# Performance work log

Hardware: AMD Instinct MI355X
Metric: run time of the kernel (lower is better)

The kernel has to match this reference:

```python
import jax, jax.numpy as jnp
import numpy as np

NE, EW, TOP_K, T_D, MAXNNZ = 32, 2944, 4, 8, 256
ALPHA, LIMIT, ORIG = 1.702, 7.0, 2880
HID = 2048


def setup_inputs() -> dict:
    key = jax.random.key(0)
    ks = jax.random.split(key, 7)
    dt = jnp.float16
    hid = jax.random.normal(ks[0], (1, 1024, HID), dtype=dt)
    # rand_init() sets all params to torch.rand(...)/5 -> Uniform[0, 0.2)
    gate_w = (jax.random.uniform(ks[1], (NE, HID), dtype=dt) * 0.2).astype(dt)
    u = (jax.random.uniform(ks[2], (NE * EW, HID), dtype=dt) * 0.2).astype(dt)
    g = (jax.random.uniform(ks[3], (NE * EW, HID), dtype=dt) * 0.2).astype(dt)
    d = (jax.random.uniform(ks[4], (HID, NE * EW), dtype=dt) * 0.2).astype(dt)
    ub = (jax.random.uniform(ks[5], (NE * EW,), dtype=dt) * 0.2).astype(dt)
    gb = (jax.random.uniform(ks[6], (NE * EW,), dtype=dt) * 0.2).astype(dt)
    return {"hid": hid, "gate_w": gate_w, "u": u, "g": g, "d": d, "ub": ub, "gb": gb}


def _act(up, gate):
    # clamped GLU: gate clamped above, up clamped both sides; glu = g*sigmoid(alpha*g); (up+1)*glu
    gate = jnp.minimum(gate, LIMIT)
    up = jnp.clip(up, -LIMIT, LIMIT)
    glu = gate * jax.nn.sigmoid(gate * ALPHA)
    act = (up + 1.0) * glu
    return act.at[..., ORIG:].set(0)  # padded inter dims (2880..2944) zeroed


def _forward(hid, gate_w, u, g, d, ub, gb):
    B, S, H = hid.shape
    x = hid.reshape(-1, H)           # [bs, H]
    bs = x.shape[0]

    # --- routing: softmax -> top-k -> renormalize -> scatter to sparse weights ---
    logits = (x @ gate_w.T).astype(jnp.float32)          # [bs, NE]
    probs = jax.nn.softmax(logits, axis=1)
    vals, idx = jax.lax.top_k(probs, TOP_K)
    vals = vals / vals.sum(axis=1, keepdims=True)
    sparse_rw = jnp.zeros_like(probs).at[jnp.arange(bs)[:, None], idx].set(vals)
    rw = sparse_rw.astype(x.dtype)                        # [bs, NE]

    # --- expert selection: t_d dense experts + t_d sparse experts by load ---
    routing_n = jnp.count_nonzero(rw, axis=0)
    mask_c = jax.lax.top_k(routing_n, 2 * T_D)[1]         # [2*T_D]
    cd, cs = mask_c[:T_D], mask_c[T_D:]
    # top-MAXNNZ tokens per sparse expert
    mask_r = jax.lax.top_k(sparse_rw[:, cs].T, MAXNNZ)[1].T  # [MAXNNZ, T_D]

    U = u.reshape(NE, EW, H)
    G = g.reshape(NE, EW, H)
    UB = ub.reshape(NE, EW)
    GB = gb.reshape(NE, EW)
    D = d.reshape(H, NE, EW)

    # --- dense experts: every token runs through the t_d hottest experts ---
    up_d = jnp.einsum('nh,teh->nte', x, U[cd]) + UB[cd]   # [bs, T_D, EW]
    gt_d = jnp.einsum('nh,teh->nte', x, G[cd]) + GB[cd]
    act_d = _act(up_d, gt_d) * rw[:, cd][..., None]       # routing weight combine
    out = jnp.einsum('nte,hte->nh', act_d, D[:, cd])      # [bs, H]

    # --- sparse experts: gather top-MAXNNZ tokens, MLP, scatter-add back ---
    xs = x[mask_r]                                        # [M, T_D, H]
    up_s = jnp.einsum('mth,teh->mte', xs, U[cs]) + UB[cs]
    gt_s = jnp.einsum('mth,teh->mte', xs, G[cs]) + GB[cs]
    w_s = rw[mask_r, cs[None, :]]                         # [M, T_D]
    act_s = _act(up_s, gt_s) * w_s[..., None]
    contrib = jnp.einsum('mte,hte->mth', act_s, D[:, cs])  # [M, T_D, H]
    out = out.at[mask_r.reshape(-1)].add(contrib.reshape(-1, H))

    return out.reshape(B, S, H)


def reference(hid, gate_w, u, g, d, ub, gb):
    return _forward(hid, gate_w, u, g, d, ub, gb)
```

## Files before the change

kernel.cpp:

```cpp
#include <hip/hip_runtime.h>

#define HID 2048
#define NE_ 32
#define EW_ 2944
#define ORIG_ 2880
#define TOPK_ 4
#define MAXNNZ_ 256
#define BS_ 1024
#define NEWTOT (NE_*EW_)
#define LDSP 40

typedef unsigned short u16;
typedef _Float16 h8  __attribute__((ext_vector_type(8)));
typedef float  f32x4 __attribute__((ext_vector_type(4)));
typedef float  fv4   __attribute__((ext_vector_type(4)));

__device__ __forceinline__ u16 f2h_bits(float f){
  union{ _Float16 h; u16 u; } c; c.h = (_Float16)f; return c.u;
}
__device__ __forceinline__ float h2f_bits(u16 u){
  union{ _Float16 h; u16 u; } c; c.u = u; return (float)c.h;
}
__device__ __forceinline__ float f16q(float f){ return (float)(_Float16)f; }

__device__ __forceinline__ h8 cvt8(fv4 a, fv4 b){
  h8 r;
  r[0]=(_Float16)a[0]; r[1]=(_Float16)a[1]; r[2]=(_Float16)a[2]; r[3]=(_Float16)a[3];
  r[4]=(_Float16)b[0]; r[5]=(_Float16)b[1]; r[6]=(_Float16)b[2]; r[7]=(_Float16)b[3];
  return r;
}
__device__ __forceinline__ int ldsx(int row, int q8){ return row*LDSP + q8*8; }

__global__ __launch_bounds__(256) void k_xcvt(const float* __restrict__ x,
                                              u16* __restrict__ xh)
{
  const int base = (blockIdx.x*256 + threadIdx.x)*8;
  fv4 a = *(const fv4*)(x+base), b = *(const fv4*)(x+base+4);
  *(h8*)(xh+base) = cvt8(a,b);
}

__global__ __launch_bounds__(256) void k_gate(const float* __restrict__ x,
                                              const float* __restrict__ gw,
                                              float* __restrict__ rw,
                                              float* __restrict__ rwf,
                                              int* __restrict__ counts)
{
  __shared__ float slog[4][NE_];
  const int tid = threadIdx.x, wid = tid>>6, lane = tid&63;
  const int n = blockIdx.x*4 + wid;
  const float* xr = x + (size_t)n*HID + lane*32;
  float xf[32];
  #pragma unroll
  for (int i=0;i<8;i++){
    fv4 v = *(const fv4*)(xr + i*4);
    #pragma unroll
    for (int j=0;j<4;j++) xf[i*4+j] = v[j];
  }
  for (int e=0;e<NE_;e++){
    const float* gr = gw + (size_t)e*HID + lane*32;
    float p = 0.f;
    #pragma unroll
    for (int i=0;i<8;i++){
      fv4 v = *(const fv4*)(gr + i*4);
      #pragma unroll
      for (int j=0;j<4;j++) p += xf[i*4+j]*v[j];
    }
    #pragma unroll
    for (int s=32;s>0;s>>=1) p += __shfl_xor(p, s);
    if (lane==0) slog[wid][e] = f16q(p);
  }
  if (lane==0){
    float mx=-1e30f;
    for (int e=0;e<NE_;e++) mx = fmaxf(mx, slog[wid][e]);
    float pr[NE_]; float sum=0.f;
    for (int e=0;e<NE_;e++){ float v=__expf(slog[wid][e]-mx); pr[e]=v; sum+=v; }
    for (int e=0;e<NE_;e++) pr[e] = pr[e]/sum;
    int   idx[TOPK_]; float val[TOPK_]; bool used[NE_];
    for (int e=0;e<NE_;e++) used[e]=false;
    float vs=0.f;
    for (int k=0;k<TOPK_;k++){
      float best=-1.f; int bi=0;
      for (int e=0;e<NE_;e++) if(!used[e] && pr[e]>best){best=pr[e];bi=e;}
      used[bi]=true; idx[k]=bi; val[k]=best; vs+=best;
    }
    float* rwr  = rw  + (size_t)n*NE_;
    float* rwfr = rwf + (size_t)n*NE_;
    for (int k=0;k<TOPK_;k++){
      float vraw = val[k]/vs;
      float q = f16q(vraw);
      rwr[idx[k]]  = q;
      rwfr[idx[k]] = vraw;
      if (q!=0.f) atomicAdd(counts+idx[k], 1);
    }
  }
}

__global__ void k_rank(const int* __restrict__ counts, int* __restrict__ cdcs)
{
  if (threadIdx.x==0){
    int cnt[NE_]; bool used[NE_];
    for (int e=0;e<NE_;e++){ cnt[e]=counts[e]; used[e]=false; }
    for (int k=0;k<16;k++){
      int best=-1, bi=0;
      for (int e=0;e<NE_;e++) if(!used[e] && cnt[e]>best){best=cnt[e];bi=e;}
      used[bi]=true; cdcs[k]=bi;
    }
  }
}

__global__ __launch_bounds__(256) void k_lists(const float* __restrict__ rw,
                                               const float* __restrict__ rwf,
                                               const int* __restrict__ cdcs,
                                               int* __restrict__ tok_all,
                                               int* __restrict__ cnt_all,
                                               int* __restrict__ inv,
                                               int* __restrict__ invcnt)
{
  __shared__ float v[BS_];
  __shared__ int scnt;
  const int z = blockIdx.x;
  const int e = cdcs[z];
  const int tid = threadIdx.x;
  for (int i=tid;i<BS_;i+=256) tok_all[z*BS_+i] = 0;
  for (int i=tid;i<BS_;i+=256) v[i] = (z<8) ? rw[(size_t)i*NE_+e] : rwf[(size_t)i*NE_+e];
  if (tid==0) scnt = 0;
  __syncthreads();
  for (int i=tid;i<BS_;i+=256){
    bool take;
    if (z<8){
      take = (v[i]!=0.f);
    } else {
      float vi=v[i]; int r=0;
      for (int m=0;m<BS_;m++){
        float vm=v[m];
        r += (vm>vi) || (vm==vi && m<i);
      }
      take = (r<MAXNNZ_) && (rw[(size_t)i*NE_+e]!=0.f);
    }
    if (take){
      int slot = atomicAdd(&scnt,1);
      tok_all[z*BS_+slot] = i;
      int c = atomicAdd(&invcnt[i],1);
      inv[i*4+c] = (z<<16) | slot;
    }
  }
  __syncthreads();
  if (tid==0) cnt_all[z] = scnt;
}

__global__ __launch_bounds__(256) void k_fused(const u16* __restrict__ xh,
                                               const float* __restrict__ uw,
                                               const float* __restrict__ gww,
                                               const float* __restrict__ ub,
                                               const float* __restrict__ gb,
                                               const float* __restrict__ rw,
                                               const int* __restrict__ cdcs,
                                               const int* __restrict__ tok_all,
                                               const int* __restrict__ cnt_all,
                                               u16* __restrict__ act)
{
  const int z=blockIdx.z, bx=blockIdx.x, by=blockIdx.y;
  const int cnt = cnt_all[z];
  if (by*256 >= cnt) return;
  const int e = cdcs[z];
  __shared__ __align__(16) u16 ldsA[2][256*LDSP];
  __shared__ __align__(16) u16 ldsB[2][64*LDSP];
  const int tid=threadIdx.x, lane=tid&63, w=tid>>6;

  const int ar = tid>>2, ach = tid&3;
  const u16* ap[4];
  #pragma unroll
  for (int r=0;r<4;r++){
    const int tok = tok_all[z*BS_ + by*256 + ar + r*64];
    ap[r] = xh + (size_t)tok*HID + ach*8;
  }
  const int br = tid>>2;
  const float* bp = (br<32 ? uw  + ((size_t)e*EW_ + bx*32 + br)*HID
                           : gww + ((size_t)e*EW_ + bx*32 + (br-32))*HID) + ach*8;

  f32x4 au[4][2], ag[4][2];
  #pragma unroll
  for (int i=0;i<4;i++)
    #pragma unroll
    for (int j=0;j<2;j++)
      #pragma unroll
      for (int q=0;q<4;q++){ au[i][j][q]=0.f; ag[i][j][q]=0.f; }

  h8 rA[4];
  #pragma unroll
  for (int r=0;r<4;r++) rA[r] = *(const h8*)ap[r];
  fv4 rB0=*(const fv4*)bp, rB1=*(const fv4*)(bp+4);
  const int NK = HID/32;
  for (int kt=0; kt<NK; kt++){
    u16* A = ldsA[kt&1]; u16* B = ldsB[kt&1];
    #pragma unroll
    for (int r=0;r<4;r++) *(h8*)&A[ldsx(ar + r*64, ach)] = rA[r];
    *(h8*)&B[ldsx(br, ach)] = cvt8(rB0,rB1);
    if (kt+1<NK){
      const int k1=(kt+1)*32;
      #pragma unroll
      for (int r=0;r<4;r++) rA[r] = *(const h8*)(ap[r]+k1);
      rB0=*(const fv4*)(bp+k1); rB1=*(const fv4*)(bp+k1+4);
    }
    __syncthreads();
    const int kq = lane>>4;
    const u16* Ar = ldsA[kt&1]; const u16* Br = ldsB[kt&1];
    h8 af[4], fu[2], fg[2];
    #pragma unroll
    for (int m=0;m<4;m++) af[m] = *(const h8*)&Ar[ldsx(w*64+m*16+(lane&15), kq)];
    #pragma unroll
    for (int n2=0;n2<2;n2++){
      fu[n2] = *(const h8*)&Br[ldsx(n2*16+(lane&15), kq)];
      fg[n2] = *(const h8*)&Br[ldsx(32+n2*16+(lane&15), kq)];
    }
    #pragma unroll
    for (int m=0;m<4;m++)
      #pragma unroll
      for (int n2=0;n2<2;n2++){
        au[m][n2]=__builtin_amdgcn_mfma_f32_16x16x32_f16(af[m],fu[n2],au[m][n2],0,0,0);
        ag[m][n2]=__builtin_amdgcn_mfma_f32_16x16x32_f16(af[m],fg[n2],ag[m][n2],0,0,0);
      }
  }

  #pragma unroll
  for (int n2=0;n2<2;n2++){
    const int col = bx*32 + n2*16 + (lane&15);
    const float ubv = ub[(size_t)e*EW_ + col];
    const float gbv = gb[(size_t)e*EW_ + col];
    #pragma unroll
    for (int m=0;m<4;m++){
      #pragma unroll
      for (int j=0;j<4;j++){
        const int s = by*256 + w*64 + m*16 + (lane>>4)*4 + j;
        if (s < cnt){
          float upv = f16q(au[m][n2][j] + ubv);
          float gtv = f16q(ag[m][n2][j] + gbv);
          float wv = rw[(size_t)tok_all[z*BS_+s]*NE_ + e];
          float gc = fminf(gtv, 7.0f);
          float uc = fminf(fmaxf(upv,-7.0f),7.0f);
          float glu = gc * (1.f/(1.f+__expf(-gc*1.702f)));
          act[((size_t)z*BS_+s)*ORIG_ + col] = f2h_bits((uc+1.f)*glu*wv);
        }
      }
    }
  }
}

__global__ __launch_bounds__(256) void k_down(const u16* __restrict__ act,
                                              const float* __restrict__ dw,
                                              const int* __restrict__ cdcs,
                                              const int* __restrict__ cnt_all,
                                              u16* __restrict__ contrib)
{
  const int zz=blockIdx.z, bx=blockIdx.x, by=blockIdx.y;
  const int z = zz>>1, kh = zz&1;
  const int cnt = cnt_all[z];
  if (by*256 >= cnt) return;
  const int e = cdcs[z];
  __shared__ __align__(16) u16 ldsA[2][256*LDSP];
  __shared__ __align__(16) u16 ldsB[2][64*LDSP];
  const int tid=threadIdx.x, lane=tid&63, w=tid>>6;
  const int ar = tid>>2, ach = tid&3;
  const int kbase = kh*1440;

  const u16* ap[4];
  #pragma unroll
  for (int r=0;r<4;r++)
    ap[r] = act + ((size_t)z*BS_ + by*256 + ar + r*64)*ORIG_ + kbase + ach*8;
  const float* bp = dw + (size_t)(bx*64 + ar)*NEWTOT + (size_t)e*EW_ + kbase + ach*8;

  f32x4 acc[4][4];
  #pragma unroll
  for (int i=0;i<4;i++)
    #pragma unroll
    for (int j=0;j<4;j++)
      #pragma unroll
      for (int q=0;q<4;q++) acc[i][j][q]=0.f;

  h8 rA[4];
  #pragma unroll
  for (int r=0;r<4;r++) rA[r] = *(const h8*)ap[r];
  fv4 rB0=*(const fv4*)bp, rB1=*(const fv4*)(bp+4);
  const int NK = 1440/32;
  for (int kt=0; kt<NK; kt++){
    u16* A = ldsA[kt&1]; u16* B = ldsB[kt&1];
    #pragma unroll
    for (int r=0;r<4;r++) *(h8*)&A[ldsx(ar + r*64, ach)] = rA[r];
    *(h8*)&B[ldsx(ar, ach)] = cvt8(rB0,rB1);
    if (kt+1<NK){
      const int k1 = (kt+1)*32;
      #pragma unroll
      for (int r=0;r<4;r++) rA[r] = *(const h8*)(ap[r]+k1);
      rB0=*(const fv4*)(bp+k1); rB1=*(const fv4*)(bp+k1+4);
    }
    __syncthreads();
    const int kq = lane>>4;
    const u16* Ar = ldsA[kt&1]; const u16* Br = ldsB[kt&1];
    h8 af[4], bfr[4];
    #pragma unroll
    for (int m=0;m<4;m++)    af[m]  = *(const h8*)&Ar[ldsx(w*64+m*16+(lane&15), kq)];
    #pragma unroll
    for (int n2=0;n2<4;n2++) bfr[n2] = *(const h8*)&Br[ldsx(n2*16+(lane&15), kq)];
    #pragma unroll
    for (int m=0;m<4;m++)
      #pragma unroll
      for (int n2=0;n2<4;n2++)
        acc[m][n2]=__builtin_amdgcn_mfma_f32_16x16x32_f16(af[m],bfr[n2],acc[m][n2],0,0,0);
  }

  #pragma unroll
  for (int m=0;m<4;m++){
    #pragma unroll
    for (int j=0;j<4;j++){
      const int slot = by*256 + w*64 + m*16 + (lane>>4)*4 + j;
      if (slot < cnt){
        #pragma unroll
        for (int n2=0;n2<4;n2++){
          const int col = bx*64 + n2*16 + (lane&15);
          contrib[((size_t)zz*BS_ + slot)*HID + col] = f2h_bits(acc[m][n2][j]);
        }
      }
    }
  }
}

__global__ __launch_bounds__(256) void k_combine(const u16* __restrict__ contrib,
                                                 const int* __restrict__ inv,
                                                 const int* __restrict__ invcnt,
                                                 float* __restrict__ out)
{
  const int gid = blockIdx.x*256 + threadIdx.x;
  const int base = gid*8;
  const int n = base >> 11;
  const int h = base & 2047;
  float acc[8];
  #pragma unroll
  for (int q=0;q<8;q++) acc[q]=0.f;
  const int c = invcnt[n];
  for (int j=0;j<c;j++){
    const int code = inv[n*4+j];
    const int z = code>>16;
    const int slot = code & 0xFFFF;
    const u16* p = contrib + ((size_t)(z*2)*BS_ + slot)*HID + h;
    h8 v0 = *(const h8*)p;
    h8 v1 = *(const h8*)(p + (size_t)BS_*HID);
    #pragma unroll
    for (int q=0;q<8;q++) acc[q] += (float)v0[q] + (float)v1[q];
  }
  fv4 o0, o1;
  #pragma unroll
  for (int q=0;q<4;q++){ o0[q]=acc[q]; o1[q]=acc[4+q]; }
  *(fv4*)(out + base) = o0;
  *(fv4*)(out + base + 4) = o1;
}

extern "C" void kernel_launch(void* const* d_in, const int* in_sizes, int n_in,
                              void* d_out, int out_size, void* d_ws, size_t ws_size,
                              hipStream_t stream)
{
  const float* x  = (const float*)d_in[0];
  const float* gw = (const float*)d_in[1];
  const float* u  = (const float*)d_in[2];
  const float* g  = (const float*)d_in[3];
  const float* dw = (const float*)d_in[4];
  const float* ub = (const float*)d_in[5];
  const float* gb = (const float*)d_in[6];

  char* ws = (char*)d_ws;
  size_t off = 0;
  auto alloc = [&](size_t bytes)->void*{ void* p = ws + off; off += (bytes + 255) & ~(size_t)255; return p; };
  float* rw     = (float*)alloc((size_t)BS_*NE_*4);
  float* rwf    = (float*)alloc((size_t)BS_*NE_*4);
  int*   counts = (int*)  alloc(NE_*4);
  int*   invcnt = (int*)  alloc(BS_*4);
  size_t zero_span = off;
  int*   cdcs   = (int*)  alloc(16*4);
  int*   cnt_all= (int*)  alloc(16*4);
  int*   tok_all= (int*)  alloc((size_t)16*BS_*4);
  int*   inv    = (int*)  alloc((size_t)BS_*4*4);
  u16*   xh     = (u16*)  alloc((size_t)BS_*HID*2);
  u16*   act    = (u16*)  alloc((size_t)16*BS_*ORIG_*2);
  u16*   contrib= (u16*)  alloc((size_t)32*BS_*HID*2);
  if (off > ws_size) return;

  hipMemsetAsync(ws, 0, zero_span, stream);

  k_xcvt <<<BS_*HID/(256*8), 256, 0, stream>>>(x, xh);
  k_gate <<<BS_/4, 256, 0, stream>>>(x, gw, rw, rwf, counts);
  k_rank <<<1,     64,  0, stream>>>(counts, cdcs);
  k_lists<<<16,    256, 0, stream>>>(rw, rwf, cdcs, tok_all, cnt_all, inv, invcnt);

  k_fused<<<dim3(ORIG_/32, 4, 16), 256, 0, stream>>>(xh, u, g, ub, gb, rw,
                                                     cdcs, tok_all, cnt_all, act);
  k_down <<<dim3(HID/64, 4, 32), 256, 0, stream>>>(act, dw, cdcs, cnt_all, contrib);
  k_combine<<<BS_*HID/(256*8), 256, 0, stream>>>(contrib, inv, invcnt, (float*)d_out);
}
```

Baseline: 575.0 us.

## Load A tiles directly into LDS with swizzle and deepen B prefetch

The A operand (fp16 activations/tokens) in both the fused up/gate GEMM and the down GEMM is now copied from global memory straight into LDS with global_load_lds, skipping registers. The LDS layout is unpadded with an XOR swizzle on 16-byte chunks to avoid bank conflicts. The fp32 B weights get a two-deep register prefetch, and the barrier moves to the top of the loop. The aim is to cut VGPR pressure and ds_write traffic and hide more load latency. The risk is synchronisation: nothing explicitly waits for the async LDS loads (no vmcnt wait) before the barrier, so correctness relies on the compiler inserting one.

Measured after the change: 582.3 us. No clear change (+1.3%).

```diff
diff --git a/kernel.cpp b/kernel.cpp
--- a/kernel.cpp
+++ b/kernel.cpp
@@ -18,9 +18,6 @@
 __device__ __forceinline__ u16 f2h_bits(float f){
   union{ _Float16 h; u16 u; } c; c.h = (_Float16)f; return c.u;
 }
-__device__ __forceinline__ float h2f_bits(u16 u){
-  union{ _Float16 h; u16 u; } c; c.u = u; return (float)c.h;
-}
 __device__ __forceinline__ float f16q(float f){ return (float)(_Float16)f; }
 
 __device__ __forceinline__ h8 cvt8(fv4 a, fv4 b){
@@ -29,7 +26,10 @@
   r[4]=(_Float16)b[0]; r[5]=(_Float16)b[1]; r[6]=(_Float16)b[2]; r[7]=(_Float16)b[3];
   return r;
 }
-__device__ __forceinline__ int ldsx(int row, int q8){ return row*LDSP + q8*8; }
+__device__ __forceinline__ void gload16(const void* g, void* l){
+  __builtin_amdgcn_global_load_lds((const __attribute__((address_space(1))) void*)g,
+                                   (__attribute__((address_space(3))) void*)l, 16, 0, 0);
+}
 
 __global__ __launch_bounds__(256) void k_xcvt(const float* __restrict__ x,
                                               u16* __restrict__ xh)
@@ -163,16 +163,16 @@
   const int cnt = cnt_all[z];
   if (by*256 >= cnt) return;
   const int e = cdcs[z];
-  __shared__ __align__(16) u16 ldsA[2][256*LDSP];
+  __shared__ __align__(16) u16 ldsA[2][256*32];
   __shared__ __align__(16) u16 ldsB[2][64*LDSP];
   const int tid=threadIdx.x, lane=tid&63, w=tid>>6;
-
   const int ar = tid>>2, ach = tid&3;
+  const int swc = ach ^ (ar&3);
   const u16* ap[4];
   #pragma unroll
   for (int r=0;r<4;r++){
     const int tok = tok_all[z*BS_ + by*256 + ar + r*64];
-    ap[r] = xh + (size_t)tok*HID + ach*8;
+    ap[r] = xh + (size_t)tok*HID + swc*8;
   }
   const int br = tid>>2;
   const float* bp = (br<32 ? uw  + ((size_t)e*EW_ + bx*32 + br)*HID
@@ -186,32 +186,37 @@
       #pragma unroll
       for (int q=0;q<4;q++){ au[i][j][q]=0.f; ag[i][j][q]=0.f; }
 
-  h8 rA[4];
-  #pragma unroll
-  for (int r=0;r<4;r++) rA[r] = *(const h8*)ap[r];
-  fv4 rB0=*(const fv4*)bp, rB1=*(const fv4*)(bp+4);
   const int NK = HID/32;
+  #pragma unroll
+  for (int r=0;r<4;r++) gload16(ap[r], &ldsA[0][(r*64 + 16*w)*32]);
+  fv4 s0a=*(const fv4*)bp,      s0b=*(const fv4*)(bp+4);
+  fv4 s1a=*(const fv4*)(bp+32), s1b=*(const fv4*)(bp+36);
+  *(h8*)&ldsB[0][br*LDSP + ach*8] = cvt8(s0a,s0b);
+  s0a=*(const fv4*)(bp+64); s0b=*(const fv4*)(bp+68);
+
   for (int kt=0; kt<NK; kt++){
-    u16* A = ldsA[kt&1]; u16* B = ldsB[kt&1];
-    #pragma unroll
-    for (int r=0;r<4;r++) *(h8*)&A[ldsx(ar + r*64, ach)] = rA[r];
-    *(h8*)&B[ldsx(br, ach)] = cvt8(rB0,rB1);
+    __syncthreads();
+    const int cur=kt&1, nxt=cur^1;
     if (kt+1<NK){
       const int k1=(kt+1)*32;
-      #pragma unroll
-      for (int r=0;r<4;r++) rA[r] = *(const h8*)(ap[r]+k1);
-      rB0=*(const fv4*)(bp+k1); rB1=*(const fv4*)(bp+k1+4);
-    }
-    __syncthreads();
+      if (((kt+1)&1)==0) *(h8*)&ldsB[nxt][br*LDSP + ach*8] = cvt8(s0a,s0b);
+      else               *(h8*)&ldsB[nxt][br*LDSP + ach*8] = cvt8(s1a,s1b);
+      #pragma unroll
+      for (int r=0;r<4;r++) gload16(ap[r]+k1, &ldsA[nxt][(r*64 + 16*w)*32]);
+      const int k3 = (kt+3<NK ? kt+3 : NK-1)*32;
+      if (((kt+1)&1)==0){ s0a=*(const fv4*)(bp+k3); s0b=*(const fv4*)(bp+k3+4); }
+      else              { s1a=*(const fv4*)(bp+k3); s1b=*(const fv4*)(bp+k3+4); }
+    }
     const int kq = lane>>4;
-    const u16* Ar = ldsA[kt&1]; const u16* Br = ldsB[kt&1];
+    const int rch = (kq ^ (lane&3))*8;
     h8 af[4], fu[2], fg[2];
     #pragma unroll
-    for (int m=0;m<4;m++) af[m] = *(const h8*)&Ar[ldsx(w*64+m*16+(lane&15), kq)];
+    for (int m=0;m<4;m++)
+      af[m] = *(const h8*)&ldsA[cur][(w*64+m*16+(lane&15))*32 + rch];
     #pragma unroll
     for (int n2=0;n2<2;n2++){
-      fu[n2] = *(const h8*)&Br[ldsx(n2*16+(lane&15), kq)];
-      fg[n2] = *(const h8*)&Br[ldsx(32+n2*16+(lane&15), kq)];
+      fu[n2] = *(const h8*)&ldsB[cur][(   n2*16+(lane&15))*LDSP + kq*8];
+      fg[n2] = *(const h8*)&ldsB[cur][(32+n2*16+(lane&15))*LDSP + kq*8];
     }
     #pragma unroll
     for (int m=0;m<4;m++)
@@ -257,16 +262,17 @@
   const int cnt = cnt_all[z];
   if (by*256 >= cnt) return;
   const int e = cdcs[z];
-  __shared__ __align__(16) u16 ldsA[2][256*LDSP];
+  __shared__ __align__(16) u16 ldsA[2][256*32];
   __shared__ __align__(16) u16 ldsB[2][64*LDSP];
   const int tid=threadIdx.x, lane=tid&63, w=tid>>6;
   const int ar = tid>>2, ach = tid&3;
+  const int swc = ach ^ (ar&3);
   const int kbase = kh*1440;
 
   const u16* ap[4];
   #pragma unroll
   for (int r=0;r<4;r++)
-    ap[r] = act + ((size_t)z*BS_ + by*256 + ar + r*64)*ORIG_ + kbase + ach*8;
+    ap[r] = act + ((size_t)z*BS_ + by*256 + ar + r*64)*ORIG_ + kbase + swc*8;
   const float* bp = dw + (size_t)(bx*64 + ar)*NEWTOT + (size_t)e*EW_ + kbase + ach*8;
 
   f32x4 acc[4][4];
@@ -277,30 +283,36 @@
       #pragma unroll
       for (int q=0;q<4;q++) acc[i][j][q]=0.f;
 
-  h8 rA[4];
-  #pragma unroll
-  for (int r=0;r<4;r++) rA[r] = *(const h8*)ap[r];
-  fv4 rB0=*(const fv4*)bp, rB1=*(const fv4*)(bp+4);
   const int NK = 1440/32;
+  #pragma unroll
+  for (int r=0;r<4;r++) gload16(ap[r], &ldsA[0][(r*64 + 16*w)*32]);
+  fv4 s0a=*(const fv4*)bp,      s0b=*(const fv4*)(bp+4);
+  fv4 s1a=*(const fv4*)(bp+32), s1b=*(const fv4*)(bp+36);
+  *(h8*)&ldsB[0][ar*LDSP + ach*8] = cvt8(s0a,s0b);
+  s0a=*(const fv4*)(bp+64); s0b=*(const fv4*)(bp+68);
+
   for (int kt=0; kt<NK; kt++){
-    u16* A = ldsA[kt&1]; u16* B = ldsB[kt&1];
-    #pragma unroll
-    for (int r=0;r<4;r++) *(h8*)&A[ldsx(ar + r*64, ach)] = rA[r];
-    *(h8*)&B[ldsx(ar, ach)] = cvt8(rB0,rB1);
+    __syncthreads();
+    const int cur=kt&1, nxt=cur^1;
     if (kt+1<NK){
-      const int k1 = (kt+1)*32;
-      #pragma unroll
-      for (int r=0;r<4;r++) rA[r] = *(const h8*)(ap[r]+k1);
-      rB0=*(const fv4*)(bp+k1); rB1=*(const fv4*)(bp+k1+4);
-    }
-    __syncthreads();
+      const int k1=(kt+1)*32;
+      if (((kt+1)&1)==0) *(h8*)&ldsB[nxt][ar*LDSP + ach*8] = cvt8(s0a,s0b);
+      else               *(h8*)&ldsB[nxt][ar*LDSP + ach*8] = cvt8(s1a,s1b);
+      #pragma unroll
+      for (int r=0;r<4;r++) gload16(ap[r]+k1, &ldsA[nxt][(r*64 + 16*w)*32]);
+      const int k3 = (kt+3<NK ? kt+3 : NK-1)*32;
+      if (((kt+1)&1)==0){ s0a=*(const fv4*)(bp+k3); s0b=*(const fv4*)(bp+k3+4); }
+      else              { s1a=*(const fv4*)(bp+k3); s1b=*(const fv4*)(bp+k3+4); }
+    }
     const int kq = lane>>4;
-    const u16* Ar = ldsA[kt&1]; const u16* Br = ldsB[kt&1];
+    const int rch = (kq ^ (lane&3))*8;
     h8 af[4], bfr[4];
     #pragma unroll
-    for (int m=0;m<4;m++)    af[m]  = *(const h8*)&Ar[ldsx(w*64+m*16+(lane&15), kq)];
-    #pragma unroll
-    for (int n2=0;n2<4;n2++) bfr[n2] = *(const h8*)&Br[ldsx(n2*16+(lane&15), kq)];
+    for (int m=0;m<4;m++)
+      af[m] = *(const h8*)&ldsA[cur][(w*64+m*16+(lane&15))*32 + rch];
+    #pragma unroll
+    for (int n2=0;n2<4;n2++)
+      bfr[n2] = *(const h8*)&ldsB[cur][(n2*16+(lane&15))*LDSP + kq*8];
     #pragma unroll
     for (int m=0;m<4;m++)
       #pragma unroll
```

## Load MFMA fragments directly from global memory, dropping LDS staging and barriers

Applied to the files above, without the earlier changes.

Both the fused up/gate GEMM and the down-projection GEMM stop staging tiles through double-buffered shared memory. Each lane now loads its own MFMA fragments straight from global memory into registers, prefetching the next k-step in registers, and the per-step __syncthreads goes away. Previously the weight tile was loaded once per block and shared by all four waves through LDS. Now each wave fetches it itself, so weight reads from L2/global rise about fourfold in exchange for removing barriers and LDS traffic.

Result: slower. 985.2 us (+71.4%).

```diff
diff --git a/kernel.cpp b/kernel.cpp
--- a/kernel.cpp
+++ b/kernel.cpp
@@ -8,7 +8,6 @@
 #define MAXNNZ_ 256
 #define BS_ 1024
 #define NEWTOT (NE_*EW_)
-#define LDSP 40
 
 typedef unsigned short u16;
 typedef _Float16 h8  __attribute__((ext_vector_type(8)));
@@ -17,9 +16,6 @@
 
 __device__ __forceinline__ u16 f2h_bits(float f){
   union{ _Float16 h; u16 u; } c; c.h = (_Float16)f; return c.u;
-}
-__device__ __forceinline__ float h2f_bits(u16 u){
-  union{ _Float16 h; u16 u; } c; c.u = u; return (float)c.h;
 }
 __device__ __forceinline__ float f16q(float f){ return (float)(_Float16)f; }
 
@@ -29,7 +25,6 @@
   r[4]=(_Float16)b[0]; r[5]=(_Float16)b[1]; r[6]=(_Float16)b[2]; r[7]=(_Float16)b[3];
   return r;
 }
-__device__ __forceinline__ int ldsx(int row, int q8){ return row*LDSP + q8*8; }
 
 __global__ __launch_bounds__(256) void k_xcvt(const float* __restrict__ x,
                                               u16* __restrict__ xh)
@@ -163,20 +158,17 @@
   const int cnt = cnt_all[z];
   if (by*256 >= cnt) return;
   const int e = cdcs[z];
-  __shared__ __align__(16) u16 ldsA[2][256*LDSP];
-  __shared__ __align__(16) u16 ldsB[2][64*LDSP];
   const int tid=threadIdx.x, lane=tid&63, w=tid>>6;
-
-  const int ar = tid>>2, ach = tid&3;
-  const u16* ap[4];
-  #pragma unroll
-  for (int r=0;r<4;r++){
-    const int tok = tok_all[z*BS_ + by*256 + ar + r*64];
-    ap[r] = xh + (size_t)tok*HID + ach*8;
-  }
-  const int br = tid>>2;
-  const float* bp = (br<32 ? uw  + ((size_t)e*EW_ + bx*32 + br)*HID
-                           : gww + ((size_t)e*EW_ + bx*32 + (br-32))*HID) + ach*8;
+  const int lr = lane&15, kq = lane>>4;
+
+  const u16* aptr[4];
+  #pragma unroll
+  for (int m=0;m<4;m++){
+    const int s = by*256 + w*64 + m*16 + lr;
+    aptr[m] = xh + (size_t)tok_all[z*BS_ + s]*HID + kq*8;
+  }
+  const float* up_ = uw  + ((size_t)e*EW_ + bx*32 + lr)*HID + kq*8;
+  const float* gp_ = gww + ((size_t)e*EW_ + bx*32 + lr)*HID + kq*8;
 
   f32x4 au[4][2], ag[4][2];
   #pragma unroll
@@ -186,52 +178,56 @@
       #pragma unroll
       for (int q=0;q<4;q++){ au[i][j][q]=0.f; ag[i][j][q]=0.f; }
 
-  h8 rA[4];
-  #pragma unroll
-  for (int r=0;r<4;r++) rA[r] = *(const h8*)ap[r];
-  fv4 rB0=*(const fv4*)bp, rB1=*(const fv4*)(bp+4);
+  h8 aC[4], uC[2], gC[2];
+  #pragma unroll
+  for (int m=0;m<4;m++) aC[m] = *(const h8*)aptr[m];
+  #pragma unroll
+  for (int n2=0;n2<2;n2++){
+    const size_t ro = (size_t)n2*16*HID;
+    uC[n2] = cvt8(*(const fv4*)(up_+ro), *(const fv4*)(up_+ro+4));
+    gC[n2] = cvt8(*(const fv4*)(gp_+ro), *(const fv4*)(gp_+ro+4));
+  }
+
   const int NK = HID/32;
+  #pragma unroll 2
   for (int kt=0; kt<NK; kt++){
-    u16* A = ldsA[kt&1]; u16* B = ldsB[kt&1];
-    #pragma unroll
-    for (int r=0;r<4;r++) *(h8*)&A[ldsx(ar + r*64, ach)] = rA[r];
-    *(h8*)&B[ldsx(br, ach)] = cvt8(rB0,rB1);
+    h8 aN[4], uN[2], gN[2];
     if (kt+1<NK){
       const int k1=(kt+1)*32;
       #pragma unroll
-      for (int r=0;r<4;r++) rA[r] = *(const h8*)(ap[r]+k1);
-      rB0=*(const fv4*)(bp+k1); rB1=*(const fv4*)(bp+k1+4);
-    }
-    __syncthreads();
-    const int kq = lane>>4;
-    const u16* Ar = ldsA[kt&1]; const u16* Br = ldsB[kt&1];
-    h8 af[4], fu[2], fg[2];
-    #pragma unroll
-    for (int m=0;m<4;m++) af[m] = *(const h8*)&Ar[ldsx(w*64+m*16+(lane&15), kq)];
-    #pragma unroll
-    for (int n2=0;n2<2;n2++){
-      fu[n2] = *(const h8*)&Br[ldsx(n2*16+(lane&15), kq)];
-      fg[n2] = *(const h8*)&Br[ldsx(32+n2*16+(lane&15), kq)];
+      for (int m=0;m<4;m++) aN[m] = *(const h8*)(aptr[m]+k1);
+      #pragma unroll
+      for (int n2=0;n2<2;n2++){
+        const size_t ro = (size_t)n2*16*HID + k1;
+        uN[n2] = cvt8(*(const fv4*)(up_+ro), *(const fv4*)(up_+ro+4));
+        gN[n2] = cvt8(*(const fv4*)(gp_+ro), *(const fv4*)(gp_+ro+4));
+      }
     }
     #pragma unroll
     for (int m=0;m<4;m++)
       #pragma unroll
       for (int n2=0;n2<2;n2++){
-        au[m][n2]=__builtin_amdgcn_mfma_f32_16x16x32_f16(af[m],fu[n2],au[m][n2],0,0,0);
-        ag[m][n2]=__builtin_amdgcn_mfma_f32_16x16x32_f16(af[m],fg[n2],ag[m][n2],0,0,0);
-      }
+        au[m][n2]=__builtin_amdgcn_mfma_f32_16x16x32_f16(aC[m],uC[n2],au[m][n2],0,0,0);
+        ag[m][n2]=__builtin_amdgcn_mfma_f32_16x16x32_f16(aC[m],gC[n2],ag[m][n2],0,0,0);
+      }
+    if (kt+1<NK){
+      #pragma unroll
+      for (int m=0;m<4;m++) aC[m]=aN[m];
+      #pragma unroll
+      for (int n2=0;n2<2;n2++){ uC[n2]=uN[n2]; gC[n2]=gN[n2]; }
+    }
   }
 
   #pragma unroll
   for (int n2=0;n2<2;n2++){
-    const int col = bx*32 + n2*16 + (lane&15);
+    const int col = bx*32 + n2*16 + lr;
     const float ubv = ub[(size_t)e*EW_ + col];
     const float gbv = gb[(size_t)e*EW_ + col];
     #pragma unroll
     for (int m=0;m<4;m++){
       #pragma unroll
       for (int j=0;j<4;j++){
-        const int s = by*256 + w*64 + m*16 + (lane>>4)*4 + j;
+        const int s = by*256 + w*64 + m*16 + kq*4 + j;
         if (s < cnt){
           float upv = f16q(au[m][n2][j] + ubv);
           float gtv = f16q(ag[m][n2][j] + gbv);
@@ -257,17 +253,15 @@
   const int cnt = cnt_all[z];
   if (by*256 >= cnt) return;
   const int e = cdcs[z];
-  __shared__ __align__(16) u16 ldsA[2][256*LDSP];
-  __shared__ __align__(16) u16 ldsB[2][64*LDSP];
   const int tid=threadIdx.x, lane=tid&63, w=tid>>6;
-  const int ar = tid>>2, ach = tid&3;
+  const int lr = lane&15, kq = lane>>4;
   const int kbase = kh*1440;
 
-  const u16* ap[4];
-  #pragma unroll
-  for (int r=0;r<4;r++)
-    ap[r] = act + ((size_t)z*BS_ + by*256 + ar + r*64)*ORIG_ + kbase + ach*8;
-  const float* bp = dw + (size_t)(bx*64 + ar)*NEWTOT + (size_t)e*EW_ + kbase + ach*8;
+  const u16* aptr[4];
+  #pragma unroll
+  for (int m=0;m<4;m++)
+    aptr[m] = act + ((size_t)z*BS_ + by*256 + w*64 + m*16 + lr)*ORIG_ + kbase + kq*8;
+  const float* bp = dw + (size_t)(bx*64 + lr)*NEWTOT + (size_t)e*EW_ + kbase + kq*8;
 
   f32x4 acc[4][4];
   #pragma unroll
@@ -277,46 +271,51 @@
       #pragma unroll
       for (int q=0;q<4;q++) acc[i][j][q]=0.f;
 
-  h8 rA[4];
-  #pragma unroll
-  for (int r=0;r<4;r++) rA[r] = *(const h8*)ap[r];
-  fv4 rB0=*(const fv4*)bp, rB1=*(const fv4*)(bp+4);
+  h8 aC[4], bC[4];
+  #pragma unroll
+  for (int m=0;m<4;m++) aC[m] = *(const h8*)aptr[m];
+  #pragma unroll
+  for (int n2=0;n2<4;n2++){
+    const size_t ro = (size_t)n2*16*NEWTOT;
+    bC[n2] = cvt8(*(const fv4*)(bp+ro), *(const fv4*)(bp+ro+4));
+  }
+
   const int NK = 1440/32;
+  #pragma unroll 2
   for (int kt=0; kt<NK; kt++){
-    u16* A = ldsA[kt&1]; u16* B = ldsB[kt&1];
-    #pragma unroll
-    for (int r=0;r<4;r++) *(h8*)&A[ldsx(ar + r*64, ach)] = rA[r];
-    *(h8*)&B[ldsx(ar, ach)] = cvt8(rB0,rB1);
+    h8 aN[4], bN[4];
     if (kt+1<NK){
       const int k1 = (kt+1)*32;
       #pragma unroll
-      for (int r=0;r<4;r++) rA[r] = *(const h8*)(ap[r]+k1);
-      rB0=*(const fv4*)(bp+k1); rB1=*(const fv4*)(bp+k1+4);
-    }
-    __syncthreads();
-    const int kq = lane>>4;
-    const u16* Ar = ldsA[kt&1]; const u16* Br = ldsB[kt&1];
-    h8 af[4], bfr[4];
-    #pragma unroll
-    for (int m=0;m<4;m++)    af[m]  = *(const h8*)&Ar[ldsx(w*64+m*16+(lane&15), kq)];
-    #pragma unroll
-    for (int n2=0;n2<4;n2++) bfr[n2] = *(const h8*)&Br[ldsx(n2*16+(lane&15), kq)];
+      for (int m=0;m<4;m++) aN[m] = *(const h8*)(aptr[m]+k1);
+      #pragma unroll
+      for (int n2=0;n2<4;n2++){
+        const size_t ro = (size_t)n2*16*NEWTOT + k1;
+        bN[n2] = cvt8(*(const fv4*)(bp+ro), *(const fv4*)(bp+ro+4));
+      }
+    }
     #pragma unroll
     for (int m=0;m<4;m++)
       #pragma unroll
       for (int n2=0;n2<4;n2++)
-        acc[m][n2]=__builtin_amdgcn_mfma_f32_16x16x32_f16(af[m],bfr[n2],acc[m][n2],0,0,0);
+        acc[m][n2]=__builtin_amdgcn_mfma_f32_16x16x32_f16(aC[m],bC[n2],acc[m][n2],0,0,0);
+    if (kt+1<NK){
+      #pragma unroll
+      for (int m=0;m<4;m++) aC[m]=aN[m];
+      #pragma unroll
+      for (int n2=0;n2<4;n2++) bC[n2]=bN[n2];
+    }
   }
 
   #pragma unroll
   for (int m=0;m<4;m++){
     #pragma unroll
     for (int j=0;j<4;j++){
-      const int slot = by*256 + w*64 + m*16 + (lane>>4)*4 + j;
+      const int slot = by*256 + w*64 + m*16 + kq*4 + j;
       if (slot < cnt){
         #pragma unroll
         for (int n2=0;n2<4;n2++){
-          const int col = bx*64 + n2*16 + (lane&15);
+          const int col = bx*64 + n2*16 + lr;
           contrib[((size_t)zz*BS_ + slot)*HID + col] = f2h_bits(acc[m][n2][j]);
         }
       }
```

## Prefetch two K-tiles ahead in register ping-pong and use lighter barriers

Applied to the files above, without the earlier changes.

Both the up/gate GEMM kernel and the down-projection GEMM kernel now hold two register sets of global loads and fetch K-tile kt+2 while tile kt is stored to LDS and multiplied. This deepens the global-load pipeline to hide memory latency. __syncthreads is replaced by an lgkmcnt wait, a raw s_barrier and a sched_barrier, so the barrier no longer waits on outstanding global loads. The cost is more registers per thread, which may lower occupancy. There is also a risk of an LDS write-after-read race, because the double buffer is reused two iterations later with only one barrier between uses.

New measurement: 576.9 us. No clear change (+0.3%).

```diff
diff --git a/kernel.cpp b/kernel.cpp
--- a/kernel.cpp
+++ b/kernel.cpp
@@ -18,9 +18,6 @@
 __device__ __forceinline__ u16 f2h_bits(float f){
   union{ _Float16 h; u16 u; } c; c.h = (_Float16)f; return c.u;
 }
-__device__ __forceinline__ float h2f_bits(u16 u){
-  union{ _Float16 h; u16 u; } c; c.u = u; return (float)c.h;
-}
 __device__ __forceinline__ float f16q(float f){ return (float)(_Float16)f; }
 
 __device__ __forceinline__ h8 cvt8(fv4 a, fv4 b){
@@ -30,6 +27,12 @@
   return r;
 }
 __device__ __forceinline__ int ldsx(int row, int q8){ return row*LDSP + q8*8; }
+
+__device__ __forceinline__ void barrier_lgkm(){
+  asm volatile("s_waitcnt lgkmcnt(0)" ::: "memory");
+  __builtin_amdgcn_s_barrier();
+  __builtin_amdgcn_sched_barrier(0);
+}
 
 __global__ __launch_bounds__(256) void k_xcvt(const float* __restrict__ x,
                                               u16* __restrict__ xh)
@@ -166,7 +169,6 @@
   __shared__ __align__(16) u16 ldsA[2][256*LDSP];
   __shared__ __align__(16) u16 ldsB[2][64*LDSP];
   const int tid=threadIdx.x, lane=tid&63, w=tid>>6;
-
   const int ar = tid>>2, ach = tid&3;
   const u16* ap[4];
   #pragma unroll
@@ -174,7 +176,7 @@
     const int tok = tok_all[z*BS_ + by*256 + ar + r*64];
     ap[r] = xh + (size_t)tok*HID + ach*8;
   }
-  const int br = tid>>2;
+  const int br = ar;
   const float* bp = (br<32 ? uw  + ((size_t)e*EW_ + bx*32 + br)*HID
                            : gww + ((size_t)e*EW_ + bx*32 + (br-32))*HID) + ach*8;
 
@@ -186,32 +188,46 @@
       #pragma unroll
       for (int q=0;q<4;q++){ au[i][j][q]=0.f; ag[i][j][q]=0.f; }
 
-  h8 rA[4];
-  #pragma unroll
-  for (int r=0;r<4;r++) rA[r] = *(const h8*)ap[r];
-  fv4 rB0=*(const fv4*)bp, rB1=*(const fv4*)(bp+4);
+  h8 A0[4], A1[4]; fv4 B0a,B0b,B1a,B1b;
+  #pragma unroll
+  for (int r=0;r<4;r++){ A0[r]=*(const h8*)ap[r]; A1[r]=*(const h8*)(ap[r]+32); }
+  B0a=*(const fv4*)bp;      B0b=*(const fv4*)(bp+4);
+  B1a=*(const fv4*)(bp+32); B1b=*(const fv4*)(bp+36);
+
   const int NK = HID/32;
+  #pragma unroll 2
   for (int kt=0; kt<NK; kt++){
     u16* A = ldsA[kt&1]; u16* B = ldsB[kt&1];
-    #pragma unroll
-    for (int r=0;r<4;r++) *(h8*)&A[ldsx(ar + r*64, ach)] = rA[r];
-    *(h8*)&B[ldsx(br, ach)] = cvt8(rB0,rB1);
-    if (kt+1<NK){
-      const int k1=(kt+1)*32;
-      #pragma unroll
-      for (int r=0;r<4;r++) rA[r] = *(const h8*)(ap[r]+k1);
-      rB0=*(const fv4*)(bp+k1); rB1=*(const fv4*)(bp+k1+4);
-    }
-    __syncthreads();
+    if ((kt&1)==0){
+      #pragma unroll
+      for (int r=0;r<4;r++) *(h8*)&A[ldsx(ar + r*64, ach)] = A0[r];
+      *(h8*)&B[ldsx(br, ach)] = cvt8(B0a,B0b);
+      if (kt+2<NK){
+        const int k2=(kt+2)*32;
+        #pragma unroll
+        for (int r=0;r<4;r++) A0[r]=*(const h8*)(ap[r]+k2);
+        B0a=*(const fv4*)(bp+k2); B0b=*(const fv4*)(bp+k2+4);
+      }
+    } else {
+      #pragma unroll
+      for (int r=0;r<4;r++) *(h8*)&A[ldsx(ar + r*64, ach)] = A1[r];
+      *(h8*)&B[ldsx(br, ach)] = cvt8(B1a,B1b);
+      if (kt+2<NK){
+        const int k2=(kt+2)*32;
+        #pragma unroll
+        for (int r=0;r<4;r++) A1[r]=*(const h8*)(ap[r]+k2);
+        B1a=*(const fv4*)(bp+k2); B1b=*(const fv4*)(bp+k2+4);
+      }
+    }
+    barrier_lgkm();
     const int kq = lane>>4;
-    const u16* Ar = ldsA[kt&1]; const u16* Br = ldsB[kt&1];
     h8 af[4], fu[2], fg[2];
     #pragma unroll
-    for (int m=0;m<4;m++) af[m] = *(const h8*)&Ar[ldsx(w*64+m*16+(lane&15), kq)];
+    for (int m=0;m<4;m++) af[m] = *(const h8*)&A[ldsx(w*64+m*16+(lane&15), kq)];
     #pragma unroll
     for (int n2=0;n2<2;n2++){
-      fu[n2] = *(const h8*)&Br[ldsx(n2*16+(lane&15), kq)];
-      fg[n2] = *(const h8*)&Br[ldsx(32+n2*16+(lane&15), kq)];
+      fu[n2] = *(const h8*)&B[ldsx(   n2*16+(lane&15), kq)];
+      fg[n2] = *(const h8*)&B[ldsx(32+n2*16+(lane&15), kq)];
     }
     #pragma unroll
     for (int m=0;m<4;m++)
@@ -277,30 +293,44 @@
       #pragma unroll
       for (int q=0;q<4;q++) acc[i][j][q]=0.f;
 
-  h8 rA[4];
-  #pragma unroll
-  for (int r=0;r<4;r++) rA[r] = *(const h8*)ap[r];
-  fv4 rB0=*(const fv4*)bp, rB1=*(const fv4*)(bp+4);
+  h8 A0[4], A1[4]; fv4 B0a,B0b,B1a,B1b;
+  #pragma unroll
+  for (int r=0;r<4;r++){ A0[r]=*(const h8*)ap[r]; A1[r]=*(const h8*)(ap[r]+32); }
+  B0a=*(const fv4*)bp;      B0b=*(const fv4*)(bp+4);
+  B1a=*(const fv4*)(bp+32); B1b=*(const fv4*)(bp+36);
+
   const int NK = 1440/32;
+  #pragma unroll 2
   for (int kt=0; kt<NK; kt++){
     u16* A = ldsA[kt&1]; u16* B = ldsB[kt&1];
-    #pragma unroll
-    for (int r=0;r<4;r++) *(h8*)&A[ldsx(ar + r*64, ach)] = rA[r];
-    *(h8*)&B[ldsx(ar, ach)] = cvt8(rB0,rB1);
-    if (kt+1<NK){
-      const int k1 = (kt+1)*32;
-      #pragma unroll
-      for (int r=0;r<4;r++) rA[r] = *(const h8*)(ap[r]+k1);
-      rB0=*(const fv4*)(bp+k1); rB1=*(const fv4*)(bp+k1+4);
-    }
-    __syncthreads();
+    if ((kt&1)==0){
+      #pragma unroll
+      for (int r=0;r<4;r++) *(h8*)&A[ldsx(ar + r*64, ach)] = A0[r];
+      *(h8*)&B[ldsx(ar, ach)] = cvt8(B0a,B0b);
+      if (kt+2<NK){
+        const int k2=(kt+2)*32;
+        #pragma unroll
+        for (int r=0;r<4;r++) A0[r]=*(const h8*)(ap[r]+k2);
+        B0a=*(const fv4*)(bp+k2); B0b=*(const fv4*)(bp+k2+4);
+      }
+    } else {
+      #pragma unroll
+      for (int r=0;r<4;r++) *(h8*)&A[ldsx(ar + r*64, ach)] = A1[r];
+      *(h8*)&B[ldsx(ar, ach)] = cvt8(B1a,B1b);
+      if (kt+2<NK){
+        const int k2=(kt+2)*32;
+        #pragma unroll
+        for (int r=0;r<4;r++) A1[r]=*(const h8*)(ap[r]+k2);
+        B1a=*(const fv4*)(bp+k2); B1b=*(const fv4*)(bp+k2+4);
+      }
+    }
+    barrier_lgkm();
     const int kq = lane>>4;
-    const u16* Ar = ldsA[kt&1]; const u16* Br = ldsB[kt&1];
     h8 af[4], bfr[4];
     #pragma unroll
-    for (int m=0;m<4;m++)    af[m]  = *(const h8*)&Ar[ldsx(w*64+m*16+(lane&15), kq)];
-    #pragma unroll
-    for (int n2=0;n2<4;n2++) bfr[n2] = *(const h8*)&Br[ldsx(n2*16+(lane&15), kq)];
+    for (int m=0;m<4;m++)    af[m]  = *(const h8*)&A[ldsx(w*64+m*16+(lane&15), kq)];
+    #pragma unroll
+    for (int n2=0;n2<4;n2++) bfr[n2] = *(const h8*)&B[ldsx(n2*16+(lane&15), kq)];
     #pragma unroll
     for (int m=0;m<4;m++)
       #pragma unroll
```
